# Performance work log

Measured on AMD Instinct MI355X. Metric: run time of the kernel, lower is better.

Reference implementation:

```python
import jax, jax.numpy as jnp
import numpy as np

ALPHA = 10.0
K = 10
BN_EPS = 1e-5


def _conv3d(x, w, b, pad):
    # x: [N,C,D,H,W], w: [O,I,kd,kh,kw]
    y = jax.lax.conv_general_dilated(
        x, w, window_strides=(1, 1, 1),
        padding=[(pad, pad)] * 3,
        dimension_numbers=('NCDHW', 'OIDHW', 'NCDHW'))
    return y + b[None, :, None, None, None]


def _bn(x, gamma, beta, mean, var):
    c = (None, slice(None), None, None, None)
    return gamma[c] * (x - mean[c]) * jax.lax.rsqrt(var[c] + BN_EPS) + beta[c]


def setup_inputs() -> dict:
    key = jax.random.key(0)
    ks = jax.random.split(key, 12)
    B, D, H, W = 1, 32, 32, 32
    LAT = 8
    M = 4096  # stored database vectors
    inp = {
        'bg_prob': jax.random.uniform(ks[0], (B, 1, D, H, W), jnp.float32),
        'ed_prob': jax.random.uniform(ks[1], (B, 1, D, H, W), jnp.float32),
        'context_mask': jnp.ones((B, D, H, W), dtype=bool),
        # conv1: 2 -> 16, k3
        'w1': jax.random.normal(ks[2], (16, 2, 3, 3, 3), jnp.float32) * 0.1,
        'b1': jnp.zeros((16,), jnp.float32),
        'g1': jnp.ones((16,), jnp.float32),
        'be1': jnp.zeros((16,), jnp.float32),
        'm1': jnp.zeros((16,), jnp.float32),
        'v1': jnp.ones((16,), jnp.float32),
        # conv2: 16 -> 32, k3
        'w2': jax.random.normal(ks[3], (32, 16, 3, 3, 3), jnp.float32) * 0.05,
        'b2': jnp.zeros((32,), jnp.float32),
        'g2': jnp.ones((32,), jnp.float32),
        'be2': jnp.zeros((32,), jnp.float32),
        'm2': jnp.zeros((32,), jnp.float32),
        'v2': jnp.ones((32,), jnp.float32),
        # conv3: 32 -> latent_dim, k1
        'w3': jax.random.normal(ks[4], (LAT, 32, 1, 1, 1), jnp.float32) * 0.1,
        'b3': jnp.zeros((LAT,), jnp.float32),
    }
    db = jax.random.normal(ks[5], (M, LAT), jnp.float32)
    db = db / jnp.maximum(jnp.linalg.norm(db, axis=1, keepdims=True), 1e-12)
    inp['db_feats'] = db
    inp['db_labels'] = jax.random.uniform(ks[6], (M,), jnp.float32)
    return inp


def reference(bg_prob, ed_prob, context_mask,
              w1, b1, g1, be1, m1, v1,
              w2, b2, g2, be2, m2, v2,
              w3, b3, db_feats, db_labels):
    # --- query encoder (BatchNorm in inference mode) ---
    x = jnp.concatenate([bg_prob, ed_prob], axis=1)              # [B,2,D,H,W]
    x = jax.nn.relu(_bn(_conv3d(x, w1, b1, 1), g1, be1, m1, v1))
    x = jax.nn.relu(_bn(_conv3d(x, w2, b2, 1), g2, be2, m2, v2))
    lat = _conv3d(x, w3, b3, 0)                                   # [B,C,D,H,W]
    # F.normalize(dim=1), eps=1e-12
    lat = lat / jnp.maximum(jnp.linalg.norm(lat, axis=1, keepdims=True), 1e-12)
    B, C, D, H, W = lat.shape
    q = lat.transpose(0, 2, 3, 4, 1).reshape(-1, C)               # [N,C]
    # --- exact L2 kNN (FAISS IndexFlatL2 returns squared distances) ---
    d2 = (jnp.sum(q * q, axis=1, keepdims=True)
          + jnp.sum(db_feats * db_feats, axis=1)[None, :]
          - 2.0 * q @ db_feats.T)                                 # [N,M]
    neg_top, idx = jax.lax.top_k(-d2, K)                          # k smallest
    dists = -neg_top                                              # [N,K]
    w = jnp.exp(-ALPHA * dists)
    lbl = db_labels[idx]                                          # [N,K] gather
    pred = jnp.sum(w * lbl, axis=1) / (jnp.sum(w, axis=1) + 1e-8)
    # NOTE: original view(B,2,D,H,W) is inconsistent (N=B*D*H*W preds);
    # return the consistent [B,D,H,W].
    return pred.reshape(B, D, H, W)
```

## Files before the change

kernel.cpp:

```cpp
#include <hip/hip_runtime.h>

#define ALPHA 10.0f
#define BN_EPS 1e-5f
#define NVOX 32768
#define MDB 4096
#define CAP 128

typedef __attribute__((ext_vector_type(8))) short short8;
typedef __attribute__((ext_vector_type(16))) float f32x16;

__device__ __forceinline__ unsigned short bfr(float x) {
  unsigned u = __float_as_uint(x);
  return (unsigned short)((u + 0x7FFFu + ((u >> 16) & 1u)) >> 16);
}
__device__ __forceinline__ void split3(float x, unsigned short& h,
                                       unsigned short& m, unsigned short& l) {
  h = bfr(x);
  float fh = __uint_as_float((unsigned)h << 16);
  float x1 = x - fh;
  m = bfr(x1);
  float fm = __uint_as_float((unsigned)m << 16);
  l = bfr(x1 - fm);
}

__device__ __forceinline__ f32x16 d2_tile(short8 a1, short8 a2, short8 a3,
                                          short8 a4, short8 b1, short8 b3,
                                          short8 b4) {
  f32x16 acc = {};
  acc = __builtin_amdgcn_mfma_f32_32x32x16_bf16(a4, b4, acc, 0, 0, 0);
  acc = __builtin_amdgcn_mfma_f32_32x32x16_bf16(a3, b3, acc, 0, 0, 0);
  acc = __builtin_amdgcn_mfma_f32_32x32x16_bf16(a2, b1, acc, 0, 0, 0);
  acc = __builtin_amdgcn_mfma_f32_32x32x16_bf16(a1, b1, acc, 0, 0, 0);
  return acc;
}

__device__ __forceinline__ float fmin3(float a, float b, float c) {
  return fminf(fminf(a, b), c);
}

#define INSERT2(d, va, vb)                                              \
  do {                                                                  \
    float _lo = fminf((va), (vb)), _hi = fmaxf((va), (vb));             \
    _Pragma("unroll")                                                   \
    for (int _k = 9; _k >= 2; --_k)                                     \
      d[_k] = fmin3(d[_k], fmaxf(d[_k - 1], _lo), fmaxf(d[_k - 2], _hi)); \
    d[1] = fmin3(d[1], fmaxf(d[0], _lo), _hi);                          \
    d[0] = fminf(d[0], _lo);                                            \
  } while (0)

__global__ __launch_bounds__(256) void k_conv1p(
    const float* __restrict__ bg, const float* __restrict__ ed,
    const float* __restrict__ w1, const float* __restrict__ b1,
    const float* __restrict__ g1, const float* __restrict__ be1,
    const float* __restrict__ m1, const float* __restrict__ v1,
    float* __restrict__ A, const float* __restrict__ db,
    const float* __restrict__ labels, unsigned short* __restrict__ DBH,
    unsigned short* __restrict__ DBM, unsigned short* __restrict__ DBL,
    unsigned short* __restrict__ DB4, unsigned* __restrict__ LBL2) {
  int t = threadIdx.x;
  if (blockIdx.x >= 128) {
    int j = (blockIdx.x - 128) * 256 + t;
    float4 x0 = ((const float4*)(db + (size_t)j * 8))[0];
    float4 x1 = ((const float4*)(db + (size_t)j * 8))[1];
    float x[8] = {x0.x, x0.y, x0.z, x0.w, x1.x, x1.y, x1.z, x1.w};
    float ss = x[0] * x[0];
#pragma unroll
    for (int i = 1; i < 8; ++i) ss = fmaf(x[i], x[i], ss);
    short8 sh = {}, sm = {}, sl = {};
#pragma unroll
    for (int i = 0; i < 8; ++i) {
      unsigned short h, m, l;
      split3(-2.f * x[i], h, m, l);
      sh[i] = (short)h; sm[i] = (short)m; sl[i] = (short)l;
    }
    unsigned short dh, dm, dl;
    split3(ss, dh, dm, dl);
    short8 s4 = {};
    s4[0] = (short)dh; s4[1] = (short)dm; s4[2] = (short)dl;
    s4[3] = (short)0x3F80; s4[4] = (short)0x3F80; s4[5] = (short)0x3F80;
    *(short8*)(DBH + (size_t)j * 8) = sh;
    *(short8*)(DBM + (size_t)j * 8) = sm;
    *(short8*)(DBL + (size_t)j * 8) = sl;
    *(short8*)(DB4 + (size_t)j * 8) = s4;
    float lb = labels[j];
    unsigned short lh = bfr(lb);
    float lf = __uint_as_float((unsigned)lh << 16);
    unsigned short ll = bfr(lb - lf);
    LBL2[j] = (unsigned)lh | ((unsigned)ll << 16);
    return;
  }
  __shared__ float wT[54 * 16];
  __shared__ float sc[16], shs[16];
  for (int i = t; i < 864; i += 256) {
    int o = i & 15, r = i >> 4;
    wT[i] = w1[o * 54 + r];
  }
  if (t < 16) {
    float s = g1[t] * rsqrtf(v1[t] + BN_EPS);
    sc[t] = s;
    shs[t] = (b1[t] - m1[t]) * s + be1[t];
  }
  __syncthreads();
  int v = blockIdx.x * 256 + t;
  int x = v & 31, y = (v >> 5) & 31, z = v >> 10;
  float acc[16];
#pragma unroll
  for (int o = 0; o < 16; ++o) acc[o] = 0.f;
#pragma unroll 1
  for (int k = 0; k < 27; ++k) {
    int dz = k / 9 - 1, dy = (k / 3) % 3 - 1, dx = k % 3 - 1;
    int zz = z + dz, yy = y + dy, xx = x + dx;
    bool inb = (unsigned)zz < 32u && (unsigned)yy < 32u && (unsigned)xx < 32u;
    int vv = zz * 1024 + yy * 32 + xx;
#pragma unroll
    for (int c = 0; c < 2; ++c) {
      const float* in = c ? ed : bg;
      float val = inb ? in[vv] : 0.f;
      const float4* wp = (const float4*)&wT[(c * 27 + k) * 16];
      float4 wa = wp[0], wb = wp[1], wc = wp[2], wd = wp[3];
      acc[0] = fmaf(val, wa.x, acc[0]);  acc[1] = fmaf(val, wa.y, acc[1]);
      acc[2] = fmaf(val, wa.z, acc[2]);  acc[3] = fmaf(val, wa.w, acc[3]);
      acc[4] = fmaf(val, wb.x, acc[4]);  acc[5] = fmaf(val, wb.y, acc[5]);
      acc[6] = fmaf(val, wb.z, acc[6]);  acc[7] = fmaf(val, wb.w, acc[7]);
      acc[8] = fmaf(val, wc.x, acc[8]);  acc[9] = fmaf(val, wc.y, acc[9]);
      acc[10] = fmaf(val, wc.z, acc[10]); acc[11] = fmaf(val, wc.w, acc[11]);
      acc[12] = fmaf(val, wd.x, acc[12]); acc[13] = fmaf(val, wd.y, acc[13]);
      acc[14] = fmaf(val, wd.z, acc[14]); acc[15] = fmaf(val, wd.w, acc[15]);
    }
  }
#pragma unroll
  for (int o = 0; o < 16; ++o) {
    float y2 = fmaf(acc[o], sc[o], shs[o]);
    A[o * NVOX + v] = y2 > 0.f ? y2 : 0.f;
  }
}

__global__ __launch_bounds__(256) void k_conv2(
    const float* __restrict__ A, const float* __restrict__ w2,
    const float* __restrict__ b2, const float* __restrict__ g2,
    const float* __restrict__ be2, const float* __restrict__ m2,
    const float* __restrict__ v2, float* __restrict__ B) {
  __shared__ float wT[432 * 8];
  __shared__ float sc[8], shs[8];
  int t = threadIdx.x;
  int og = blockIdx.x >> 7;
  int vb = blockIdx.x & 127;
  for (int i = t; i < 3456; i += 256) {
    int o = i & 7, r = i >> 3;
    wT[i] = w2[(og * 8 + o) * 432 + r];
  }
  if (t < 8) {
    int o = og * 8 + t;
    float s = g2[o] * rsqrtf(v2[o] + BN_EPS);
    sc[t] = s;
    shs[t] = (b2[o] - m2[o]) * s + be2[o];
  }
  __syncthreads();
  int v = vb * 256 + t;
  int x = v & 31, y = (v >> 5) & 31, z = v >> 10;
  float acc[8];
#pragma unroll
  for (int o = 0; o < 8; ++o) acc[o] = 0.f;
#pragma unroll 1
  for (int k = 0; k < 27; ++k) {
    int dz = k / 9 - 1, dy = (k / 3) % 3 - 1, dx = k % 3 - 1;
    int zz = z + dz, yy = y + dy, xx = x + dx;
    bool inb = (unsigned)zz < 32u && (unsigned)yy < 32u && (unsigned)xx < 32u;
    int vv = zz * 1024 + yy * 32 + xx;
#pragma unroll
    for (int ci = 0; ci < 16; ++ci) {
      float val = inb ? A[ci * NVOX + vv] : 0.f;
      const float4* wp = (const float4*)&wT[(ci * 27 + k) * 8];
      float4 wa = wp[0], wb = wp[1];
      acc[0] = fmaf(val, wa.x, acc[0]); acc[1] = fmaf(val, wa.y, acc[1]);
      acc[2] = fmaf(val, wa.z, acc[2]); acc[3] = fmaf(val, wa.w, acc[3]);
      acc[4] = fmaf(val, wb.x, acc[4]); acc[5] = fmaf(val, wb.y, acc[5]);
      acc[6] = fmaf(val, wb.z, acc[6]); acc[7] = fmaf(val, wb.w, acc[7]);
    }
  }
#pragma unroll
  for (int o = 0; o < 8; ++o) {
    float y2 = fmaf(acc[o], sc[o], shs[o]);
    B[(og * 8 + o) * NVOX + v] = y2 > 0.f ? y2 : 0.f;
  }
}

__global__ __launch_bounds__(256) void k_conv3q(
    const float* __restrict__ B, const float* __restrict__ w3,
    const float* __restrict__ b3, unsigned short* __restrict__ QH,
    unsigned short* __restrict__ QM, unsigned short* __restrict__ QL,
    unsigned short* __restrict__ Q4) {
  __shared__ float wT[32 * 8];
  __shared__ float bL[8];
  int t = threadIdx.x;
  {
    int o = t & 7, ci = t >> 3;
    wT[t] = w3[o * 32 + ci];
  }
  if (t < 8) bL[t] = b3[t];
  __syncthreads();
  int v = blockIdx.x * 256 + t;
  float lat[8];
#pragma unroll
  for (int o = 0; o < 8; ++o) lat[o] = bL[o];
#pragma unroll 4
  for (int ci = 0; ci < 32; ++ci) {
    float val = B[ci * NVOX + v];
    const float4* wp = (const float4*)&wT[ci * 8];
    float4 wa = wp[0], wb = wp[1];
    lat[0] = fmaf(val, wa.x, lat[0]); lat[1] = fmaf(val, wa.y, lat[1]);
    lat[2] = fmaf(val, wa.z, lat[2]); lat[3] = fmaf(val, wa.w, lat[3]);
    lat[4] = fmaf(val, wb.x, lat[4]); lat[5] = fmaf(val, wb.y, lat[5]);
    lat[6] = fmaf(val, wb.z, lat[6]); lat[7] = fmaf(val, wb.w, lat[7]);
  }
  float n2 = 0.f;
#pragma unroll
  for (int o = 0; o < 8; ++o) n2 = fmaf(lat[o], lat[o], n2);
  float inv = 1.f / fmaxf(sqrtf(n2), 1e-12f);
  float q[8];
#pragma unroll
  for (int o = 0; o < 8; ++o) q[o] = lat[o] * inv;
  float qq = q[0] * q[0];
#pragma unroll
  for (int o = 1; o < 8; ++o) qq = fmaf(q[o], q[o], qq);
  short8 sh = {}, sm = {}, sl = {};
#pragma unroll
  for (int o = 0; o < 8; ++o) {
    unsigned short h, m, l;
    split3(q[o], h, m, l);
    sh[o] = (short)h; sm[o] = (short)m; sl[o] = (short)l;
  }
  unsigned short qh, qm, ql;
  split3(qq, qh, qm, ql);
  short8 s4 = {};
  s4[0] = (short)0x3F80; s4[1] = (short)0x3F80; s4[2] = (short)0x3F80;
  s4[3] = (short)qh; s4[4] = (short)qm; s4[5] = (short)ql;
  *(short8*)(QH + (size_t)v * 8) = sh;
  *(short8*)(QM + (size_t)v * 8) = sm;
  *(short8*)(QL + (size_t)v * 8) = sl;
  *(short8*)(Q4 + (size_t)v * 8) = s4;
}

__global__ __launch_bounds__(512) void k_knn_fused(
    const unsigned short* __restrict__ QH, const unsigned short* __restrict__ QM,
    const unsigned short* __restrict__ QL, const unsigned short* __restrict__ Q4,
    const unsigned short* __restrict__ DBH, const unsigned short* __restrict__ DBM,
    const unsigned short* __restrict__ DBL, const unsigned short* __restrict__ DB4,
    const unsigned* __restrict__ LBL2, float* __restrict__ out) {
  __shared__ float lds_top[8][10][32];
  __shared__ float T0L[32];
  __shared__ int cnt[32];
  __shared__ float listd[32][CAP + 1];
  __shared__ float listl[32][CAP + 1];
  int t = threadIdx.x, w = t >> 6, l = t & 63;
  int lo32 = l & 31, hi = l >> 5;
  int q = blockIdx.x * 32 + lo32;
  if (t < 32) cnt[t] = 0;
  short8 zz = {};
  short8 b1 = *(const short8*)((hi ? QM : QH) + (size_t)q * 8);
  short8 b3 = *(const short8*)((hi ? QL : QH) + (size_t)q * 8);
  short8 b4v = *(const short8*)(Q4 + (size_t)q * 8);
  short8 b4 = hi ? zz : b4v;
  int r0 = w * 512;

  float d[10];
#pragma unroll
  for (int k = 0; k < 10; ++k) d[k] = 3.4e38f;
#pragma unroll 1
  for (int tt = 0; tt < 4; ++tt) {
    int r = r0 + tt * 32 + lo32;
    short8 a1 = *(const short8*)(DBH + (size_t)r * 8);
    short8 a2 = *(const short8*)(DBM + (size_t)r * 8);
    short8 a3 = *(const short8*)((hi ? DBH : DBL) + (size_t)r * 8);
    short8 a4 = *(const short8*)(DB4 + (size_t)r * 8);
    f32x16 acc = d2_tile(a1, a2, a3, a4, b1, b3, b4);
#pragma unroll
    for (int p = 0; p < 8; ++p) INSERT2(d, acc[2 * p], acc[2 * p + 1]);
  }
  {
    float e[10];
#pragma unroll
    for (int k = 0; k < 10; ++k) e[k] = __shfl_xor(d[k], 32);
#pragma unroll
    for (int k = 0; k < 10; k += 2) INSERT2(d, e[k], e[k + 1]);
  }
  if (l < 32) {
#pragma unroll
    for (int k = 0; k < 10; ++k) lds_top[w][k][lo32] = d[k];
  }
  __syncthreads();
  if (t < 32) {
    float m[10];
#pragma unroll
    for (int k = 0; k < 10; ++k) m[k] = 3.4e38f;
#pragma unroll 1
    for (int w2 = 0; w2 < 8; ++w2) {
#pragma unroll
      for (int k2 = 0; k2 < 10; k2 += 2)
        INSERT2(m, lds_top[w2][k2][t], lds_top[w2][k2 + 1][t]);
    }
    T0L[t] = m[9];
  }
  __syncthreads();
  float T0q = T0L[lo32];

  short8 b_one = zz;
  if (!hi) { b_one[0] = (short)0x3F80; b_one[1] = (short)0x3F80; }
#pragma unroll 1
  for (int tt = 0; tt < 16; ++tt) {
    int r = r0 + tt * 32 + lo32;
    short8 a1 = *(const short8*)(DBH + (size_t)r * 8);
    short8 a2 = *(const short8*)(DBM + (size_t)r * 8);
    short8 a3 = *(const short8*)((hi ? DBH : DBL) + (size_t)r * 8);
    short8 a4 = *(const short8*)(DB4 + (size_t)r * 8);
    unsigned lu = LBL2[r];
    short8 a_lab = zz;
    a_lab[0] = (short)(lu & 0xFFFFu);
    a_lab[1] = (short)(lu >> 16);
    f32x16 acc = d2_tile(a1, a2, a3, a4, b1, b3, b4);
    f32x16 accL = {};
    accL = __builtin_amdgcn_mfma_f32_32x32x16_bf16(a_lab, b_one, accL, 0, 0, 0);
#pragma unroll
    for (int i = 0; i < 16; ++i) {
      float d2v = acc[i];
      bool p = d2v <= T0q;
      if (__any(p)) {
        if (p) {
          int slot = atomicAdd(&cnt[lo32], 1);
          if (slot < CAP) {
            listd[lo32][slot] = d2v;
            listl[lo32][slot] = accL[i];
          }
        }
      }
    }
  }
  __syncthreads();

  if (t < 32) {
    int n = min(cnt[t], CAP);
    float dd[10];
#pragma unroll
    for (int k = 0; k < 10; ++k) dd[k] = 3.4e38f;
    int j = 0;
#pragma unroll 1
    for (; j + 1 < n; j += 2) INSERT2(dd, listd[t][j], listd[t][j + 1]);
    if (j < n) INSERT2(dd, listd[t][j], 3.4e38f);
    float Tv = dd[9];
    const float C2 = -14.4269504088896340736f;
    float num = 0.f, den = 0.f;
#pragma unroll 1
    for (int j2 = 0; j2 < n; ++j2) {
      float v = listd[t][j2];
      if (v <= Tv) {
        float e = exp2f(v * C2);
        den += e;
        num = fmaf(e, listl[t][j2], num);
      }
    }
    out[blockIdx.x * 32 + t] = num / (den + 1e-8f);
  }
}

extern "C" void kernel_launch(void* const* d_in, const int* in_sizes, int n_in,
                              void* d_out, int out_size, void* d_ws, size_t ws_size,
                              hipStream_t stream) {
  const float* bg = (const float*)d_in[0];
  const float* ed = (const float*)d_in[1];
  const float* w1 = (const float*)d_in[3];
  const float* b1 = (const float*)d_in[4];
  const float* g1 = (const float*)d_in[5];
  const float* be1 = (const float*)d_in[6];
  const float* m1 = (const float*)d_in[7];
  const float* v1 = (const float*)d_in[8];
  const float* w2 = (const float*)d_in[9];
  const float* b2 = (const float*)d_in[10];
  const float* g2 = (const float*)d_in[11];
  const float* be2 = (const float*)d_in[12];
  const float* m2 = (const float*)d_in[13];
  const float* v2 = (const float*)d_in[14];
  const float* w3 = (const float*)d_in[15];
  const float* b3 = (const float*)d_in[16];
  const float* db = (const float*)d_in[17];
  const float* labels = (const float*)d_in[18];
  float* out = (float*)d_out;

  char* ws = (char*)d_ws;
  const size_t MB = 1024 * 1024;
  float* A = (float*)(ws + 0);
  float* B = (float*)(ws + 2 * MB);
  unsigned short* QH = (unsigned short*)(ws + 0);
  unsigned short* QM = QH + (size_t)NVOX * 8;
  unsigned short* QL = QM + (size_t)NVOX * 8;
  unsigned short* Q4 = QL + (size_t)NVOX * 8;
  unsigned short* DBH = (unsigned short*)(ws + 6 * MB);
  unsigned short* DBM = DBH + (size_t)MDB * 8;
  unsigned short* DBL = DBM + (size_t)MDB * 8;
  unsigned short* DB4 = DBL + (size_t)MDB * 8;
  unsigned* LBL2 = (unsigned*)(DB4 + (size_t)MDB * 8);

  k_conv1p<<<144, 256, 0, stream>>>(bg, ed, w1, b1, g1, be1, m1, v1, A, db,
                                    labels, DBH, DBM, DBL, DB4, LBL2);
  k_conv2<<<4 * 128, 256, 0, stream>>>(A, w2, b2, g2, be2, m2, v2, B);
  k_conv3q<<<NVOX / 256, 256, 0, stream>>>(B, w3, b3, QH, QM, QL, Q4);
  k_knn_fused<<<NVOX / 32, 512, 0, stream>>>(QH, QM, QL, Q4, DBH, DBM, DBL,
                                             DB4, LBL2, out);
}
```

Baseline: 126.1 us.

## Replace label MFMA with index-based label gather; halve conv block sizes

The kNN kernel no longer carries labels through an extra bf16 MFMA per tile. It records the database row index of each candidate and gathers the fp32 labels from global memory after the candidate scan, which also removes the label-split preprocessing and the LBL2 buffer. Shared memory is reused: the top-k staging array now aliases the candidate lists. Separately, conv1 and conv3 now launch 128-thread blocks over twice as many blocks, which should spread work across more CUs. The gather adds a scattered global read phase and an extra barrier.

```diff
diff --git a/kernel.cpp b/kernel.cpp
--- a/kernel.cpp
+++ b/kernel.cpp
@@ -48,18 +48,17 @@
     d[0] = fminf(d[0], _lo);                                            \
   } while (0)
 
-__global__ __launch_bounds__(256) void k_conv1p(
+__global__ __launch_bounds__(128) void k_conv1p(
     const float* __restrict__ bg, const float* __restrict__ ed,
     const float* __restrict__ w1, const float* __restrict__ b1,
     const float* __restrict__ g1, const float* __restrict__ be1,
     const float* __restrict__ m1, const float* __restrict__ v1,
     float* __restrict__ A, const float* __restrict__ db,
-    const float* __restrict__ labels, unsigned short* __restrict__ DBH,
-    unsigned short* __restrict__ DBM, unsigned short* __restrict__ DBL,
-    unsigned short* __restrict__ DB4, unsigned* __restrict__ LBL2) {
+    unsigned short* __restrict__ DBH, unsigned short* __restrict__ DBM,
+    unsigned short* __restrict__ DBL, unsigned short* __restrict__ DB4) {
   int t = threadIdx.x;
-  if (blockIdx.x >= 128) {
-    int j = (blockIdx.x - 128) * 256 + t;
+  if (blockIdx.x >= 256) {
+    int j = (blockIdx.x - 256) * 128 + t;
     float4 x0 = ((const float4*)(db + (size_t)j * 8))[0];
     float4 x1 = ((const float4*)(db + (size_t)j * 8))[1];
     float x[8] = {x0.x, x0.y, x0.z, x0.w, x1.x, x1.y, x1.z, x1.w};
@@ -82,16 +81,11 @@
     *(short8*)(DBM + (size_t)j * 8) = sm;
     *(short8*)(DBL + (size_t)j * 8) = sl;
     *(short8*)(DB4 + (size_t)j * 8) = s4;
-    float lb = labels[j];
-    unsigned short lh = bfr(lb);
-    float lf = __uint_as_float((unsigned)lh << 16);
-    unsigned short ll = bfr(lb - lf);
-    LBL2[j] = (unsigned)lh | ((unsigned)ll << 16);
     return;
   }
   __shared__ float wT[54 * 16];
   __shared__ float sc[16], shs[16];
-  for (int i = t; i < 864; i += 256) {
+  for (int i = t; i < 864; i += 128) {
     int o = i & 15, r = i >> 4;
     wT[i] = w1[o * 54 + r];
   }
@@ -101,7 +95,7 @@
     shs[t] = (b1[t] - m1[t]) * s + be1[t];
   }
   __syncthreads();
-  int v = blockIdx.x * 256 + t;
+  int v = blockIdx.x * 128 + t;
   int x = v & 31, y = (v >> 5) & 31, z = v >> 10;
   float acc[16];
 #pragma unroll
@@ -185,7 +179,7 @@
   }
 }
 
-__global__ __launch_bounds__(256) void k_conv3q(
+__global__ __launch_bounds__(128) void k_conv3q(
     const float* __restrict__ B, const float* __restrict__ w3,
     const float* __restrict__ b3, unsigned short* __restrict__ QH,
     unsigned short* __restrict__ QM, unsigned short* __restrict__ QL,
@@ -193,13 +187,13 @@
   __shared__ float wT[32 * 8];
   __shared__ float bL[8];
   int t = threadIdx.x;
-  {
-    int o = t & 7, ci = t >> 3;
-    wT[t] = w3[o * 32 + ci];
+  for (int i = t; i < 256; i += 128) {
+    int o = i & 7, ci = i >> 3;
+    wT[i] = w3[o * 32 + ci];
   }
   if (t < 8) bL[t] = b3[t];
   __syncthreads();
-  int v = blockIdx.x * 256 + t;
+  int v = blockIdx.x * 128 + t;
   float lat[8];
 #pragma unroll
   for (int o = 0; o < 8; ++o) lat[o] = bL[o];
@@ -246,12 +240,13 @@
     const unsigned short* __restrict__ QL, const unsigned short* __restrict__ Q4,
     const unsigned short* __restrict__ DBH, const unsigned short* __restrict__ DBM,
     const unsigned short* __restrict__ DBL, const unsigned short* __restrict__ DB4,
-    const unsigned* __restrict__ LBL2, float* __restrict__ out) {
-  __shared__ float lds_top[8][10][32];
+    const float* __restrict__ labels, float* __restrict__ out) {
+  __shared__ float smem[2 * 32 * (CAP + 1)];
   __shared__ float T0L[32];
   __shared__ int cnt[32];
-  __shared__ float listd[32][CAP + 1];
-  __shared__ float listl[32][CAP + 1];
+  float (*listd)[CAP + 1] = (float (*)[CAP + 1])smem;
+  int (*listi)[CAP + 1] = (int (*)[CAP + 1])(smem + 32 * (CAP + 1));
+  float (*lds_top)[10][32] = (float (*)[10][32])smem;
   int t = threadIdx.x, w = t >> 6, l = t & 63;
   int lo32 = l & 31, hi = l >> 5;
   int q = blockIdx.x * 32 + lo32;
@@ -304,8 +299,6 @@
   __syncthreads();
   float T0q = T0L[lo32];
 
-  short8 b_one = zz;
-  if (!hi) { b_one[0] = (short)0x3F80; b_one[1] = (short)0x3F80; }
 #pragma unroll 1
   for (int tt = 0; tt < 16; ++tt) {
     int r = r0 + tt * 32 + lo32;
@@ -313,13 +306,8 @@
     short8 a2 = *(const short8*)(DBM + (size_t)r * 8);
     short8 a3 = *(const short8*)((hi ? DBH : DBL) + (size_t)r * 8);
     short8 a4 = *(const short8*)(DB4 + (size_t)r * 8);
-    unsigned lu = LBL2[r];
-    short8 a_lab = zz;
-    a_lab[0] = (short)(lu & 0xFFFFu);
-    a_lab[1] = (short)(lu >> 16);
     f32x16 acc = d2_tile(a1, a2, a3, a4, b1, b3, b4);
-    f32x16 accL = {};
-    accL = __builtin_amdgcn_mfma_f32_32x32x16_bf16(a_lab, b_one, accL, 0, 0, 0);
+    int rb = r0 + tt * 32 + 4 * hi;
 #pragma unroll
     for (int i = 0; i < 16; ++i) {
       float d2v = acc[i];
@@ -329,10 +317,20 @@
           int slot = atomicAdd(&cnt[lo32], 1);
           if (slot < CAP) {
             listd[lo32][slot] = d2v;
-            listl[lo32][slot] = accL[i];
+            listi[lo32][slot] = rb + (i & 3) + 8 * (i >> 2);
           }
         }
       }
+    }
+  }
+  __syncthreads();
+
+  {
+    int qc = t >> 4, s0 = t & 15;
+    int n = min(cnt[qc], CAP);
+    for (int s = s0; s < n; s += 16) {
+      int idx = listi[qc][s];
+      ((float*)listi[qc])[s] = labels[idx];
     }
   }
   __syncthreads();
@@ -355,7 +353,7 @@
       if (v <= Tv) {
         float e = exp2f(v * C2);
         den += e;
-        num = fmaf(e, listl[t][j2], num);
+        num = fmaf(e, ((float*)listi[t])[j2], num);
       }
     }
     out[blockIdx.x * 32 + t] = num / (den + 1e-8f);
@@ -397,12 +395,11 @@
   unsigned short* DBM = DBH + (size_t)MDB * 8;
   unsigned short* DBL = DBM + (size_t)MDB * 8;
   unsigned short* DB4 = DBL + (size_t)MDB * 8;
-  unsigned* LBL2 = (unsigned*)(DB4 + (size_t)MDB * 8);
-
-  k_conv1p<<<144, 256, 0, stream>>>(bg, ed, w1, b1, g1, be1, m1, v1, A, db,
-                                    labels, DBH, DBM, DBL, DB4, LBL2);
+
+  k_conv1p<<<288, 128, 0, stream>>>(bg, ed, w1, b1, g1, be1, m1, v1, A, db,
+                                    DBH, DBM, DBL, DB4);
   k_conv2<<<4 * 128, 256, 0, stream>>>(A, w2, b2, g2, be2, m2, v2, B);
-  k_conv3q<<<NVOX / 256, 256, 0, stream>>>(B, w3, b3, QH, QM, QL, Q4);
+  k_conv3q<<<256, 128, 0, stream>>>(B, w3, b3, QH, QM, QL, Q4);
   k_knn_fused<<<NVOX / 32, 512, 0, stream>>>(QH, QM, QL, Q4, DBH, DBM, DBL,
-                                             DB4, LBL2, out);
-}
+                                             DB4, labels, out);
+}
```

Result: faster. 115.7 us (-8.2%).
